# Kernel tuning notes

Measured on AMD Instinct MI355X. Metric: run time of the kernel, lower is better.

The kernel has to match this reference:

```python
import jax, jax.numpy as jnp
import numpy as np

EMB = 256
N = 262144
B = 512
SLOPE = 0.01  # torch LeakyReLU default negative slope


def leaky_relu(x):
    return jnp.where(x >= 0, x, SLOPE * x)


def setup_inputs() -> dict:
    key = jax.random.key(0)
    ks = jax.random.split(key, 10)
    s = 1.0 / np.sqrt(EMB)
    s2 = 1.0 / np.sqrt(2 * EMB)
    return {
        "xg_prev": jax.random.normal(ks[0], (B, EMB), jnp.float32),
        "x": jax.random.normal(ks[1], (N, EMB), jnp.float32),
        "batch_ind": jnp.sort(jax.random.randint(ks[2], (N,), 0, B)),
        "W_mask": jax.random.uniform(ks[3], (EMB, 1), jnp.float32, -s, s),
        "b_mask": jax.random.uniform(ks[4], (1,), jnp.float32, -s, s),
        "W_feat": jax.random.uniform(ks[5], (EMB, EMB), jnp.float32, -s, s),
        "b_feat": jax.random.uniform(ks[6], (EMB,), jnp.float32, -s, s),
        "W_t": jax.random.uniform(ks[7], (2 * EMB, EMB), jnp.float32, -s2, s2),
        "b_t": jax.random.uniform(ks[8], (EMB,), jnp.float32, -s2, s2),
    }


def reference(xg_prev, x, batch_ind, W_mask, b_mask, W_feat, b_feat, W_t, b_t):
    # GlobalAttention pooling (PyG): gate = att_mask(x), feat = att_feat(x)
    gate = (x @ W_mask + b_mask)[:, 0]                      # [N]
    feat = leaky_relu(x @ W_feat + b_feat)                  # [N, EMB]
    # segment-wise stable softmax over gate per graph
    seg_max = jax.ops.segment_max(gate, batch_ind, num_segments=B)  # [B]
    seg_max = jnp.where(jnp.isfinite(seg_max), seg_max, 0.0)
    e = jnp.exp(gate - seg_max[batch_ind])                  # [N]
    denom = jax.ops.segment_sum(e, batch_ind, num_segments=B)      # [B]
    w = e / jnp.maximum(denom[batch_ind], 1e-16)            # [N]
    xg = jax.ops.segment_sum(w[:, None] * feat, batch_ind, num_segments=B)  # [B, EMB]
    # concat -> linear -> leaky_relu -> residual
    h = jnp.concatenate([xg, xg_prev], axis=1)              # [B, 2*EMB]
    out = leaky_relu(h @ W_t + b_t) + xg_prev               # [B, EMB]
    return out
```

## Files before the change

### kernel.cpp

```cpp
#include <hip/hip_runtime.h>
#include <cstdint>
#include <cstddef>

#define NROWS 262144
#define EMB 256
#define NB 512
#define NCOPY 8
#define SLOPE 0.01f

typedef __attribute__((ext_vector_type(8))) short short8;
typedef __attribute__((ext_vector_type(4))) float f32x4;

__device__ __forceinline__ unsigned short f2bf(float f) {
    unsigned u = __float_as_uint(f);
    u += 0x7FFFu + ((u >> 16) & 1u);
    return (unsigned short)(u >> 16);
}

__device__ __forceinline__ short8 pack8(const float4& lo, const float4& hi) {
    short8 s;
    s[0] = (short)f2bf(lo.x); s[1] = (short)f2bf(lo.y);
    s[2] = (short)f2bf(lo.z); s[3] = (short)f2bf(lo.w);
    s[4] = (short)f2bf(hi.x); s[5] = (short)f2bf(hi.y);
    s[6] = (short)f2bf(hi.z); s[7] = (short)f2bf(hi.w);
    return s;
}

__device__ __forceinline__ void gld16f(float* l, const float* g) {
    __builtin_amdgcn_global_load_lds(
        (const __attribute__((address_space(1))) unsigned int*)g,
        (__attribute__((address_space(3))) unsigned int*)l, 16, 0, 0);
}
__device__ __forceinline__ void gld16u(unsigned short* l, const unsigned short* g) {
    __builtin_amdgcn_global_load_lds(
        (const __attribute__((address_space(1))) unsigned int*)g,
        (__attribute__((address_space(3))) unsigned int*)l, 16, 0, 0);
}

__global__ __launch_bounds__(256) void k_init(float4* xgPart4, float4* dPart4) {
    int i = blockIdx.x * 256 + threadIdx.x;
    if (i < NCOPY * NB * EMB / 4) xgPart4[i] = (float4){0.f, 0.f, 0.f, 0.f};
    else dPart4[i - NCOPY * NB * EMB / 4] = (float4){0.f, 0.f, 0.f, 0.f};
}

__global__ __launch_bounds__(256) void k_prep(const float* __restrict__ Wf,
                                              unsigned short* __restrict__ Wt2) {
    int b = blockIdx.x, t = threadIdx.x;
    float v = Wf[(size_t)b * EMB + t];
    Wt2[((size_t)(b >> 3) << 11) + (t << 3) + (b & 7)] = f2bf(v);
}

#define STAGE(B, KT) do {                                                         \
    _Pragma("unroll")                                                             \
    for (int q = 0; q < 2; q++) {                                                 \
        const int i_ = q * 512 + t;                                               \
        const int row_ = i_ >> 3, c_ = i_ & 7;                                    \
        const int cs_ = c_ ^ (row_ & 7);                                          \
        gld16f(&xbuf[B][i_ * 4], x + ((r0 + row_) << 8) + (KT) + (cs_ << 2));     \
    }                                                                             \
    _Pragma("unroll")                                                             \
    for (int q = 0; q < 2; q++) {                                                 \
        const int i_ = q * 512 + t;                                               \
        const int slab_ = i_ >> 8, off_ = i_ & 255;                               \
        gld16u(&bbuf[B][slab_ * 2048 + off_ * 8],                                 \
               Wt2 + (((size_t)((KT) >> 3) + slab_) << 11) + off_ * 8);           \
    }                                                                             \
} while (0)

__global__ __launch_bounds__(512, 4) void k_fused(const float* __restrict__ x,
                                                  const unsigned short* __restrict__ Wt2,
                                                  const float* __restrict__ wm,
                                                  const float* __restrict__ bfeat,
                                                  const int* __restrict__ bind,
                                                  float* __restrict__ dPart,
                                                  float* __restrict__ xgPart) {
    __shared__ float          xbuf[2][128 * 32];
    __shared__ unsigned short bbuf[2][32 * 256];
    __shared__ float wm_s[256];
    __shared__ float w_s[128];
    __shared__ float pxg[2][256];
    __shared__ float pden[2];
    __shared__ int   seg_s[128];
    __shared__ int   segid_s[8];
    __shared__ int   uni_s[8];

    const int t    = threadIdx.x;
    const int lane = t & 63;
    const int w    = t >> 6;
    const int wr   = w >> 1, wc = w & 1;
    const int fr   = lane & 15;
    const int fg   = lane >> 4;
    const size_t r0 = (size_t)blockIdx.x * 128;
    const int cp   = blockIdx.x & (NCOPY - 1);

    if (t < 256) { wm_s[t] = wm[t]; pxg[0][t] = 0.f; pxg[1][t] = 0.f; }
    if (t < 128) seg_s[t] = bind[r0 + t];
    if (t < 2)   pden[t] = 0.f;

    STAGE(0, 0);

    f32x4 acc[2][8];
#pragma unroll
    for (int m = 0; m < 2; m++)
#pragma unroll
        for (int n = 0; n < 8; n++) acc[m][n] = (f32x4){0.f, 0.f, 0.f, 0.f};
    float gp0 = 0.f, gp1 = 0.f;

#pragma unroll
    for (int s = 0; s < 8; s++) {
        const int buf = s & 1;
        if (s < 7) STAGE(buf ^ 1, (s + 1) * 32);
        if (s < 7) asm volatile("s_waitcnt vmcnt(4)" ::: "memory");
        else       asm volatile("s_waitcnt vmcnt(0)" ::: "memory");
        __builtin_amdgcn_sched_barrier(0);
        __builtin_amdgcn_s_barrier();
        __builtin_amdgcn_sched_barrier(0);

        const float* xb = &xbuf[buf][0];
        const unsigned short* bb = &bbuf[buf][0];

        const float4 wa  = *reinterpret_cast<const float4*>(&wm_s[s * 32 + fg * 8]);
        const float4 wbv = *reinterpret_cast<const float4*>(&wm_s[s * 32 + fg * 8 + 4]);
        short8 a0, a1;
        {
            const int r  = wr * 32 + fr;
            const int sl = (fg * 2) ^ (r & 7);
            const float4 lo = *reinterpret_cast<const float4*>(&xb[r * 32 + sl * 4]);
            const float4 hi = *reinterpret_cast<const float4*>(&xb[r * 32 + (sl ^ 1) * 4]);
            gp0 += lo.x * wa.x + lo.y * wa.y + lo.z * wa.z + lo.w * wa.w
                 + hi.x * wbv.x + hi.y * wbv.y + hi.z * wbv.z + hi.w * wbv.w;
            a0 = pack8(lo, hi);
        }
        {
            const int r  = wr * 32 + 16 + fr;
            const int sl = (fg * 2) ^ (r & 7);
            const float4 lo = *reinterpret_cast<const float4*>(&xb[r * 32 + sl * 4]);
            const float4 hi = *reinterpret_cast<const float4*>(&xb[r * 32 + (sl ^ 1) * 4]);
            gp1 += lo.x * wa.x + lo.y * wa.y + lo.z * wa.z + lo.w * wa.w
                 + hi.x * wbv.x + hi.y * wbv.y + hi.z * wbv.z + hi.w * wbv.w;
            a1 = pack8(lo, hi);
        }
#pragma unroll
        for (int n = 0; n < 8; n++) {
            const short8 b = *reinterpret_cast<const short8*>(
                &bb[fg * 2048 + ((wc * 128 + n * 16 + fr) << 3)]);
            acc[0][n] = __builtin_amdgcn_mfma_f32_16x16x32_bf16(a0, b, acc[0][n], 0, 0, 0);
            acc[1][n] = __builtin_amdgcn_mfma_f32_16x16x32_bf16(a1, b, acc[1][n], 0, 0, 0);
        }

        asm volatile("s_waitcnt lgkmcnt(0)" ::: "memory");
        __builtin_amdgcn_sched_barrier(0);
        __builtin_amdgcn_s_barrier();
        __builtin_amdgcn_sched_barrier(0);
    }

    gp0 += __shfl_xor(gp0, 16, 64); gp0 += __shfl_xor(gp0, 32, 64);
    gp1 += __shfl_xor(gp1, 16, 64); gp1 += __shfl_xor(gp1, 32, 64);
    if (wc == 0 && lane < 16) {
        w_s[wr * 32 + lane]      = expf(gp0);
        w_s[wr * 32 + 16 + lane] = expf(gp1);
    }
    if (t < 8) {
        int s0 = seg_s[t * 16], ok = 1;
#pragma unroll
        for (int i = 1; i < 16; i++) ok &= (seg_s[t * 16 + i] == s0);
        segid_s[t] = s0;
        uni_s[t]   = ok;
    }
    __syncthreads();

    const int sid0 = seg_s[0];
    const int sid1 = seg_s[127];

    if (t < 8) {
        if (uni_s[t]) {
            float s = 0.f;
#pragma unroll
            for (int i = 0; i < 16; i++) s += w_s[t * 16 + i];
            const int sid = segid_s[t];
            if (sid == sid0)      atomicAdd(&pden[0], s);
            else if (sid == sid1) atomicAdd(&pden[1], s);
            else atomicAdd(&dPart[cp * NB + sid], s);
        } else {
            for (int i = 0; i < 16; i++) {
                const int sd = seg_s[t * 16 + i];
                const float e = w_s[t * 16 + i];
                if (sd == sid0)      atomicAdd(&pden[0], e);
                else if (sd == sid1) atomicAdd(&pden[1], e);
                else atomicAdd(&dPart[cp * NB + sd], e);
            }
        }
    }

#pragma unroll
    for (int m = 0; m < 2; m++) {
        const int g    = wr * 2 + m;
        const int uni  = uni_s[g];
        const int sid  = segid_s[g];
        const int rowb = wr * 32 + m * 16;
#pragma unroll
        for (int n = 0; n < 8; n++) {
            const int col = wc * 128 + n * 16 + fr;
            const float bia = bfeat[col];
            float vr[4];
#pragma unroll
            for (int r = 0; r < 4; r++) {
                const int row = rowb + fg * 4 + r;
                float v = acc[m][n][r] + bia;
                v = (v >= 0.f) ? v : SLOPE * v;
                vr[r] = v * w_s[row];
            }
            if (uni) {
                float s = vr[0] + vr[1] + vr[2] + vr[3];
                s += __shfl_xor(s, 16, 64);
                s += __shfl_xor(s, 32, 64);
                if (fg == 0) {
                    if (sid == sid0)      atomicAdd(&pxg[0][col], s);
                    else if (sid == sid1) atomicAdd(&pxg[1][col], s);
                    else atomicAdd(&xgPart[((size_t)(cp * NB + sid) << 8) + col], s);
                }
            } else {
#pragma unroll
                for (int r = 0; r < 4; r++) {
                    const int sd = seg_s[rowb + fg * 4 + r];
                    if (sd == sid0)      atomicAdd(&pxg[0][col], vr[r]);
                    else if (sd == sid1) atomicAdd(&pxg[1][col], vr[r]);
                    else atomicAdd(&xgPart[((size_t)(cp * NB + sd) << 8) + col], vr[r]);
                }
            }
        }
    }
    __syncthreads();

    if (t < 256) {
        atomicAdd(&xgPart[((size_t)(cp * NB + sid0) << 8) + t], pxg[0][t]);
    } else if (sid1 != sid0) {
        atomicAdd(&xgPart[((size_t)(cp * NB + sid1) << 8) + (t - 256)], pxg[1][t - 256]);
    }
    if (t == 0) atomicAdd(&dPart[cp * NB + sid0], pden[0]);
    if (t == 1 && sid1 != sid0) atomicAdd(&dPart[cp * NB + sid1], pden[1]);
}

__global__ __launch_bounds__(256) void k_out(const float* __restrict__ xgPart,
                                             const float* __restrict__ dPart,
                                             const float* __restrict__ xgp,
                                             const float* __restrict__ Wtr,
                                             const float* __restrict__ bt,
                                             float* __restrict__ out) {
    __shared__ float h[8][512];
    const int c  = threadIdx.x;
    const int b0 = blockIdx.x * 8;
#pragma unroll
    for (int r = 0; r < 8; r++) {
        const int b = b0 + r;
        float den = 0.f, s = 0.f;
#pragma unroll
        for (int cpy = 0; cpy < NCOPY; cpy++) {
            den += dPart[cpy * NB + b];
            s   += xgPart[((size_t)(cpy * NB + b) << 8) + c];
        }
        h[r][c]       = s / fmaxf(den, 1e-16f);
        h[r][EMB + c] = xgp[(size_t)b * EMB + c];
    }
    __syncthreads();
    float acc[8] = {0.f, 0.f, 0.f, 0.f, 0.f, 0.f, 0.f, 0.f};
    for (int k = 0; k < 2 * EMB; k++) {
        float wv = Wtr[(size_t)k * EMB + c];
#pragma unroll
        for (int r = 0; r < 8; r++) acc[r] += h[r][k] * wv;
    }
#pragma unroll
    for (int r = 0; r < 8; r++) {
        float v = acc[r] + bt[c];
        v = (v >= 0.f) ? v : SLOPE * v;
        out[(size_t)(b0 + r) * EMB + c] = v + xgp[(size_t)(b0 + r) * EMB + c];
    }
}

extern "C" void kernel_launch(void* const* d_in, const int* in_sizes, int n_in,
                              void* d_out, int out_size, void* d_ws, size_t ws_size,
                              hipStream_t stream) {
    const float* xgp  = (const float*)d_in[0];
    const float* x    = (const float*)d_in[1];
    const int*   bind = (const int*)d_in[2];
    const float* Wm   = (const float*)d_in[3];
    const float* Wf   = (const float*)d_in[5];
    const float* bf   = (const float*)d_in[6];
    const float* Wtr  = (const float*)d_in[7];
    const float* bt   = (const float*)d_in[8];
    float* out = (float*)d_out;

    char* ws = (char*)d_ws;
    unsigned short* Wt2    = (unsigned short*)ws;
    float*          dPart  = (float*)(ws + 131072);
    float*          xgPart = (float*)(ws + 131072 + 16384);

    hipLaunchKernelGGL(k_init,  dim3(1028),        dim3(256), 0, stream,
                       (float4*)xgPart, (float4*)dPart);
    hipLaunchKernelGGL(k_prep,  dim3(256),         dim3(256), 0, stream, Wf, Wt2);
    hipLaunchKernelGGL(k_fused, dim3(NROWS / 128), dim3(512), 0, stream,
                       x, Wt2, Wm, bf, bind, dPart, xgPart);
    hipLaunchKernelGGL(k_out,   dim3(NB / 8),      dim3(256), 0, stream,
                       xgPart, dPart, xgp, Wtr, bt, out);
}
```

Before: 142.6 us.

## Load x directly into registers and halve rows per block

The x tile is no longer staged through LDS. Each lane now loads its own A fragment (8 floats per k-step) straight from global memory into registers and prefetches the next step one iteration ahead. The block tile shrinks from 128 to 64 rows, so there are twice as many blocks, and launch bounds rise to 6 blocks per SM to cut LDS and register use and raise occupancy. In exchange, the W tile in LDS is now reused across only 64 rows, so per-row W staging traffic doubles and per-block overhead such as pxg atomics and setup grows.

```diff
diff --git a/kernel.cpp b/kernel.cpp
--- a/kernel.cpp
+++ b/kernel.cpp
@@ -26,11 +26,6 @@
     return s;
 }
 
-__device__ __forceinline__ void gld16f(float* l, const float* g) {
-    __builtin_amdgcn_global_load_lds(
-        (const __attribute__((address_space(1))) unsigned int*)g,
-        (__attribute__((address_space(3))) unsigned int*)l, 16, 0, 0);
-}
 __device__ __forceinline__ void gld16u(unsigned short* l, const unsigned short* g) {
     __builtin_amdgcn_global_load_lds(
         (const __attribute__((address_space(1))) unsigned int*)g,
@@ -50,14 +45,7 @@
     Wt2[((size_t)(b >> 3) << 11) + (t << 3) + (b & 7)] = f2bf(v);
 }
 
-#define STAGE(B, KT) do {                                                         \
-    _Pragma("unroll")                                                             \
-    for (int q = 0; q < 2; q++) {                                                 \
-        const int i_ = q * 512 + t;                                               \
-        const int row_ = i_ >> 3, c_ = i_ & 7;                                    \
-        const int cs_ = c_ ^ (row_ & 7);                                          \
-        gld16f(&xbuf[B][i_ * 4], x + ((r0 + row_) << 8) + (KT) + (cs_ << 2));     \
-    }                                                                             \
+#define STAGE_B(B, KT) do {                                                       \
     _Pragma("unroll")                                                             \
     for (int q = 0; q < 2; q++) {                                                 \
         const int i_ = q * 512 + t;                                               \
@@ -67,22 +55,21 @@
     }                                                                             \
 } while (0)
 
-__global__ __launch_bounds__(512, 4) void k_fused(const float* __restrict__ x,
+__global__ __launch_bounds__(512, 6) void k_fused(const float* __restrict__ x,
                                                   const unsigned short* __restrict__ Wt2,
                                                   const float* __restrict__ wm,
                                                   const float* __restrict__ bfeat,
                                                   const int* __restrict__ bind,
                                                   float* __restrict__ dPart,
                                                   float* __restrict__ xgPart) {
-    __shared__ float          xbuf[2][128 * 32];
     __shared__ unsigned short bbuf[2][32 * 256];
     __shared__ float wm_s[256];
-    __shared__ float w_s[128];
+    __shared__ float w_s[64];
     __shared__ float pxg[2][256];
     __shared__ float pden[2];
-    __shared__ int   seg_s[128];
-    __shared__ int   segid_s[8];
-    __shared__ int   uni_s[8];
+    __shared__ int   seg_s[64];
+    __shared__ int   segid_s[4];
+    __shared__ int   uni_s[4];
 
     const int t    = threadIdx.x;
     const int lane = t & 63;
@@ -90,77 +77,64 @@
     const int wr   = w >> 1, wc = w & 1;
     const int fr   = lane & 15;
     const int fg   = lane >> 4;
-    const size_t r0 = (size_t)blockIdx.x * 128;
+    const size_t r0 = (size_t)blockIdx.x * 64;
     const int cp   = blockIdx.x & (NCOPY - 1);
 
     if (t < 256) { wm_s[t] = wm[t]; pxg[0][t] = 0.f; pxg[1][t] = 0.f; }
-    if (t < 128) seg_s[t] = bind[r0 + t];
-    if (t < 2)   pden[t] = 0.f;
-
-    STAGE(0, 0);
-
-    f32x4 acc[2][8];
-#pragma unroll
-    for (int m = 0; m < 2; m++)
-#pragma unroll
-        for (int n = 0; n < 8; n++) acc[m][n] = (f32x4){0.f, 0.f, 0.f, 0.f};
-    float gp0 = 0.f, gp1 = 0.f;
+    if (t < 64) seg_s[t] = bind[r0 + t];
+    if (t < 2)  pden[t] = 0.f;
+
+    const float* xrow = x + (r0 + wr * 16 + fr) * EMB + fg * 8;
+
+    STAGE_B(0, 0);
+    float4 aLo = *reinterpret_cast<const float4*>(xrow);
+    float4 aHi = *reinterpret_cast<const float4*>(xrow + 4);
+
+    f32x4 acc[8];
+#pragma unroll
+    for (int n = 0; n < 8; n++) acc[n] = (f32x4){0.f, 0.f, 0.f, 0.f};
+    float gp = 0.f;
 
 #pragma unroll
     for (int s = 0; s < 8; s++) {
         const int buf = s & 1;
-        if (s < 7) STAGE(buf ^ 1, (s + 1) * 32);
-        if (s < 7) asm volatile("s_waitcnt vmcnt(4)" ::: "memory");
+        float4 nLo, nHi;
+        if (s < 7) {
+            STAGE_B(buf ^ 1, (s + 1) * 32);
+            nLo = *reinterpret_cast<const float4*>(xrow + (s + 1) * 32);
+            nHi = *reinterpret_cast<const float4*>(xrow + (s + 1) * 32 + 4);
+        }
+        if (s < 7) asm volatile("s_waitcnt vmcnt(6)" ::: "memory");
         else       asm volatile("s_waitcnt vmcnt(0)" ::: "memory");
         __builtin_amdgcn_sched_barrier(0);
         __builtin_amdgcn_s_barrier();
         __builtin_amdgcn_sched_barrier(0);
-
-        const float* xb = &xbuf[buf][0];
-        const unsigned short* bb = &bbuf[buf][0];
 
         const float4 wa  = *reinterpret_cast<const float4*>(&wm_s[s * 32 + fg * 8]);
         const float4 wbv = *reinterpret_cast<const float4*>(&wm_s[s * 32 + fg * 8 + 4]);
-        short8 a0, a1;
-        {
-            const int r  = wr * 32 + fr;
-            const int sl = (fg * 2) ^ (r & 7);
-            const float4 lo = *reinterpret_cast<const float4*>(&xb[r * 32 + sl * 4]);
-            const float4 hi = *reinterpret_cast<const float4*>(&xb[r * 32 + (sl ^ 1) * 4]);
-            gp0 += lo.x * wa.x + lo.y * wa.y + lo.z * wa.z + lo.w * wa.w
-                 + hi.x * wbv.x + hi.y * wbv.y + hi.z * wbv.z + hi.w * wbv.w;
-            a0 = pack8(lo, hi);
-        }
-        {
-            const int r  = wr * 32 + 16 + fr;
-            const int sl = (fg * 2) ^ (r & 7);
-            const float4 lo = *reinterpret_cast<const float4*>(&xb[r * 32 + sl * 4]);
-            const float4 hi = *reinterpret_cast<const float4*>(&xb[r * 32 + (sl ^ 1) * 4]);
-            gp1 += lo.x * wa.x + lo.y * wa.y + lo.z * wa.z + lo.w * wa.w
-                 + hi.x * wbv.x + hi.y * wbv.y + hi.z * wbv.z + hi.w * wbv.w;
-            a1 = pack8(lo, hi);
-        }
+        gp += aLo.x * wa.x + aLo.y * wa.y + aLo.z * wa.z + aLo.w * wa.w
+            + aHi.x * wbv.x + aHi.y * wbv.y + aHi.z * wbv.z + aHi.w * wbv.w;
+        const short8 a = pack8(aLo, aHi);
+        const unsigned short* bb = &bbuf[buf][0];
 #pragma unroll
         for (int n = 0; n < 8; n++) {
             const short8 b = *reinterpret_cast<const short8*>(
                 &bb[fg * 2048 + ((wc * 128 + n * 16 + fr) << 3)]);
-            acc[0][n] = __builtin_amdgcn_mfma_f32_16x16x32_bf16(a0, b, acc[0][n], 0, 0, 0);
-            acc[1][n] = __builtin_amdgcn_mfma_f32_16x16x32_bf16(a1, b, acc[1][n], 0, 0, 0);
+            acc[n] = __builtin_amdgcn_mfma_f32_16x16x32_bf16(a, b, acc[n], 0, 0, 0);
         }
 
         asm volatile("s_waitcnt lgkmcnt(0)" ::: "memory");
         __builtin_amdgcn_sched_barrier(0);
         __builtin_amdgcn_s_barrier();
         __builtin_amdgcn_sched_barrier(0);
-    }
-
-    gp0 += __shfl_xor(gp0, 16, 64); gp0 += __shfl_xor(gp0, 32, 64);
-    gp1 += __shfl_xor(gp1, 16, 64); gp1 += __shfl_xor(gp1, 32, 64);
-    if (wc == 0 && lane < 16) {
-        w_s[wr * 32 + lane]      = expf(gp0);
-        w_s[wr * 32 + 16 + lane] = expf(gp1);
-    }
-    if (t < 8) {
+
+        aLo = nLo; aHi = nHi;
+    }
+
+    gp += __shfl_xor(gp, 16, 64);
+    gp += __shfl_xor(gp, 32, 64);
+    if (wc == 0 && lane < 16) w_s[wr * 16 + lane] = expf(gp);
+    if (t < 4) {
         int s0 = seg_s[t * 16], ok = 1;
 #pragma unroll
         for (int i = 1; i < 16; i++) ok &= (seg_s[t * 16 + i] == s0);
@@ -170,9 +144,9 @@
     __syncthreads();
 
     const int sid0 = seg_s[0];
-    const int sid1 = seg_s[127];
-
-    if (t < 8) {
+    const int sid1 = seg_s[63];
+
+    if (t < 4) {
         if (uni_s[t]) {
             float s = 0.f;
 #pragma unroll
@@ -192,12 +166,11 @@
         }
     }
 
-#pragma unroll
-    for (int m = 0; m < 2; m++) {
-        const int g    = wr * 2 + m;
+    {
+        const int g    = wr;
         const int uni  = uni_s[g];
         const int sid  = segid_s[g];
-        const int rowb = wr * 32 + m * 16;
+        const int rowb = wr * 16;
 #pragma unroll
         for (int n = 0; n < 8; n++) {
             const int col = wc * 128 + n * 16 + fr;
@@ -206,7 +179,7 @@
 #pragma unroll
             for (int r = 0; r < 4; r++) {
                 const int row = rowb + fg * 4 + r;
-                float v = acc[m][n][r] + bia;
+                float v = acc[n][r] + bia;
                 v = (v >= 0.f) ? v : SLOPE * v;
                 vr[r] = v * w_s[row];
             }
@@ -295,11 +268,11 @@
     float*          dPart  = (float*)(ws + 131072);
     float*          xgPart = (float*)(ws + 131072 + 16384);
 
-    hipLaunchKernelGGL(k_init,  dim3(1028),        dim3(256), 0, stream,
+    hipLaunchKernelGGL(k_init,  dim3(1028),       dim3(256), 0, stream,
                        (float4*)xgPart, (float4*)dPart);
-    hipLaunchKernelGGL(k_prep,  dim3(256),         dim3(256), 0, stream, Wf, Wt2);
-    hipLaunchKernelGGL(k_fused, dim3(NROWS / 128), dim3(512), 0, stream,
+    hipLaunchKernelGGL(k_prep,  dim3(256),        dim3(256), 0, stream, Wf, Wt2);
+    hipLaunchKernelGGL(k_fused, dim3(NROWS / 64), dim3(512), 0, stream,
                        x, Wt2, Wm, bf, bind, dPart, xgPart);
-    hipLaunchKernelGGL(k_out,   dim3(NB / 8),      dim3(256), 0, stream,
+    hipLaunchKernelGGL(k_out,   dim3(NB / 8),     dim3(256), 0, stream,
                        xgPart, dPart, xgp, Wtr, bt, out);
 }
```

Result: slower. 161.3 us (+13.1%).

## Stage x through registers with two-ahead prefetch and merge init/prep kernels

Applied to the files above, without the earlier changes.

Replaces the direct global-to-LDS loads of x with register loads that are fetched two k-steps ahead and written into the swizzled LDS buffer one step ahead. The weight tile still uses global_load_lds, and the vmcnt waits are retuned to match. Separately, the zeroing kernel is folded into the weight-prep kernel, which removes one launch. This raises register pressure and adds explicit LDS stores in exchange for a deeper prefetch of the dominant x stream.

```diff
diff --git a/kernel.cpp b/kernel.cpp
--- a/kernel.cpp
+++ b/kernel.cpp
@@ -26,38 +26,28 @@
     return s;
 }
 
-__device__ __forceinline__ void gld16f(float* l, const float* g) {
-    __builtin_amdgcn_global_load_lds(
-        (const __attribute__((address_space(1))) unsigned int*)g,
-        (__attribute__((address_space(3))) unsigned int*)l, 16, 0, 0);
-}
 __device__ __forceinline__ void gld16u(unsigned short* l, const unsigned short* g) {
     __builtin_amdgcn_global_load_lds(
         (const __attribute__((address_space(1))) unsigned int*)g,
         (__attribute__((address_space(3))) unsigned int*)l, 16, 0, 0);
 }
 
-__global__ __launch_bounds__(256) void k_init(float4* xgPart4, float4* dPart4) {
-    int i = blockIdx.x * 256 + threadIdx.x;
-    if (i < NCOPY * NB * EMB / 4) xgPart4[i] = (float4){0.f, 0.f, 0.f, 0.f};
-    else dPart4[i - NCOPY * NB * EMB / 4] = (float4){0.f, 0.f, 0.f, 0.f};
-}
-
 __global__ __launch_bounds__(256) void k_prep(const float* __restrict__ Wf,
-                                              unsigned short* __restrict__ Wt2) {
-    int b = blockIdx.x, t = threadIdx.x;
-    float v = Wf[(size_t)b * EMB + t];
-    Wt2[((size_t)(b >> 3) << 11) + (t << 3) + (b & 7)] = f2bf(v);
-}
-
-#define STAGE(B, KT) do {                                                         \
-    _Pragma("unroll")                                                             \
-    for (int q = 0; q < 2; q++) {                                                 \
-        const int i_ = q * 512 + t;                                               \
-        const int row_ = i_ >> 3, c_ = i_ & 7;                                    \
-        const int cs_ = c_ ^ (row_ & 7);                                          \
-        gld16f(&xbuf[B][i_ * 4], x + ((r0 + row_) << 8) + (KT) + (cs_ << 2));     \
-    }                                                                             \
+                                              unsigned short* __restrict__ Wt2,
+                                              float4* __restrict__ xgPart4,
+                                              float4* __restrict__ dPart4) {
+    const int b = blockIdx.x, t = threadIdx.x;
+    if (b < 256) {
+        float v = Wf[(size_t)b * EMB + t];
+        Wt2[((size_t)(b >> 3) << 11) + (t << 3) + (b & 7)] = f2bf(v);
+    } else {
+        const int i = (b - 256) * 256 + t;
+        if (i < NCOPY * NB * EMB / 4) xgPart4[i] = (float4){0.f, 0.f, 0.f, 0.f};
+        else dPart4[i - NCOPY * NB * EMB / 4] = (float4){0.f, 0.f, 0.f, 0.f};
+    }
+}
+
+#define STAGE_B(B, KT) do {                                                       \
     _Pragma("unroll")                                                             \
     for (int q = 0; q < 2; q++) {                                                 \
         const int i_ = q * 512 + t;                                               \
@@ -97,7 +87,28 @@
     if (t < 128) seg_s[t] = bind[r0 + t];
     if (t < 2)   pden[t] = 0.f;
 
-    STAGE(0, 0);
+    const int row0  = t >> 3, c0 = t & 7;
+    const int wslot = c0 ^ (row0 & 7);
+    const int wb0   = row0 * 32 + wslot * 4;
+    const int wb1   = wb0 + 64 * 32;
+    const float* xsrc0 = x + (r0 + row0) * EMB + c0 * 4;
+    const float* xsrc1 = xsrc0 + (size_t)64 * EMB;
+
+    float4 aLo, aHi, nLo = {}, nHi = {};
+    {
+        float4 z0 = *reinterpret_cast<const float4*>(xsrc0);
+        float4 z1 = *reinterpret_cast<const float4*>(xsrc1);
+        __builtin_amdgcn_sched_barrier(0);
+        STAGE_B(0, 0);
+        __builtin_amdgcn_sched_barrier(0);
+        aLo = *reinterpret_cast<const float4*>(xsrc0 + 32);
+        aHi = *reinterpret_cast<const float4*>(xsrc1 + 32);
+        __builtin_amdgcn_sched_barrier(0);
+        asm volatile("s_waitcnt vmcnt(4)" ::: "memory");
+        __builtin_amdgcn_sched_barrier(0);
+        *reinterpret_cast<float4*>(&xbuf[0][wb0]) = z0;
+        *reinterpret_cast<float4*>(&xbuf[0][wb1]) = z1;
+    }
 
     f32x4 acc[2][8];
 #pragma unroll
@@ -109,9 +120,22 @@
 #pragma unroll
     for (int s = 0; s < 8; s++) {
         const int buf = s & 1;
-        if (s < 7) STAGE(buf ^ 1, (s + 1) * 32);
-        if (s < 7) asm volatile("s_waitcnt vmcnt(4)" ::: "memory");
-        else       asm volatile("s_waitcnt vmcnt(0)" ::: "memory");
+        if (s < 7) STAGE_B(buf ^ 1, (s + 1) * 32);
+        __builtin_amdgcn_sched_barrier(0);
+        if (s < 6) {
+            nLo = *reinterpret_cast<const float4*>(xsrc0 + (s + 2) * 32);
+            nHi = *reinterpret_cast<const float4*>(xsrc1 + (s + 2) * 32);
+        }
+        __builtin_amdgcn_sched_barrier(0);
+        if (s < 6)       asm volatile("s_waitcnt vmcnt(4)" ::: "memory");
+        else if (s == 6) asm volatile("s_waitcnt vmcnt(2)" ::: "memory");
+        else             asm volatile("s_waitcnt vmcnt(0)" ::: "memory");
+        __builtin_amdgcn_sched_barrier(0);
+        if (s < 7) {
+            *reinterpret_cast<float4*>(&xbuf[buf ^ 1][wb0]) = aLo;
+            *reinterpret_cast<float4*>(&xbuf[buf ^ 1][wb1]) = aHi;
+        }
+        asm volatile("s_waitcnt lgkmcnt(0)" ::: "memory");
         __builtin_amdgcn_sched_barrier(0);
         __builtin_amdgcn_s_barrier();
         __builtin_amdgcn_sched_barrier(0);
@@ -152,6 +176,8 @@
         __builtin_amdgcn_sched_barrier(0);
         __builtin_amdgcn_s_barrier();
         __builtin_amdgcn_sched_barrier(0);
+
+        aLo = nLo; aHi = nHi;
     }
 
     gp0 += __shfl_xor(gp0, 16, 64); gp0 += __shfl_xor(gp0, 32, 64);
@@ -204,11 +230,11 @@
             const float bia = bfeat[col];
             float vr[4];
 #pragma unroll
-            for (int r = 0; r < 4; r++) {
-                const int row = rowb + fg * 4 + r;
-                float v = acc[m][n][r] + bia;
+            for (int r2 = 0; r2 < 4; r2++) {
+                const int row = rowb + fg * 4 + r2;
+                float v = acc[m][n][r2] + bia;
                 v = (v >= 0.f) ? v : SLOPE * v;
-                vr[r] = v * w_s[row];
+                vr[r2] = v * w_s[row];
             }
             if (uni) {
                 float s = vr[0] + vr[1] + vr[2] + vr[3];
@@ -221,11 +247,11 @@
                 }
             } else {
 #pragma unroll
-                for (int r = 0; r < 4; r++) {
-                    const int sd = seg_s[rowb + fg * 4 + r];
-                    if (sd == sid0)      atomicAdd(&pxg[0][col], vr[r]);
-                    else if (sd == sid1) atomicAdd(&pxg[1][col], vr[r]);
-                    else atomicAdd(&xgPart[((size_t)(cp * NB + sd) << 8) + col], vr[r]);
+                for (int r2 = 0; r2 < 4; r2++) {
+                    const int sd = seg_s[rowb + fg * 4 + r2];
+                    if (sd == sid0)      atomicAdd(&pxg[0][col], vr[r2]);
+                    else if (sd == sid1) atomicAdd(&pxg[1][col], vr[r2]);
+                    else atomicAdd(&xgPart[((size_t)(cp * NB + sd) << 8) + col], vr[r2]);
                 }
             }
         }
@@ -295,11 +321,10 @@
     float*          dPart  = (float*)(ws + 131072);
     float*          xgPart = (float*)(ws + 131072 + 16384);
 
-    hipLaunchKernelGGL(k_init,  dim3(1028),        dim3(256), 0, stream,
-                       (float4*)xgPart, (float4*)dPart);
-    hipLaunchKernelGGL(k_prep,  dim3(256),         dim3(256), 0, stream, Wf, Wt2);
+    hipLaunchKernelGGL(k_prep,  dim3(256 + 1028), dim3(256), 0, stream,
+                       Wf, Wt2, (float4*)xgPart, (float4*)dPart);
     hipLaunchKernelGGL(k_fused, dim3(NROWS / 128), dim3(512), 0, stream,
                        x, Wt2, Wm, bf, bind, dPart, xgPart);
-    hipLaunchKernelGGL(k_out,   dim3(NB / 8),      dim3(256), 0, stream,
+    hipLaunchKernelGGL(k_out,   dim3(NB / 8),     dim3(256), 0, stream,
                        xgPart, dPart, xgp, Wtr, bt, out);
 }
```

Result: no change. 144.5 us (+1.3%).

## Double row tile to 256 per 1024-thread block and merge init into prep

Applied to the files above, without the earlier changes.

The fused kernel now processes 256 rows per block with 1024 threads (16 waves), so each staged B tile of the bf16 weight matrix is shared by twice as many rows. This halves the weight traffic per row and halves the number of blocks and global atomic flushes. The zero-init kernel is folded into the weight-prep kernel, removing one launch. In exchange, LDS use per block roughly doubles (xbuf grows to 64 KB), which can cut residency and overlap, and launch_bounds(1024,4) may force tight register limits.

```diff
diff --git a/kernel.cpp b/kernel.cpp
--- a/kernel.cpp
+++ b/kernel.cpp
@@ -37,52 +37,52 @@
         (__attribute__((address_space(3))) unsigned int*)l, 16, 0, 0);
 }
 
-__global__ __launch_bounds__(256) void k_init(float4* xgPart4, float4* dPart4) {
-    int i = blockIdx.x * 256 + threadIdx.x;
-    if (i < NCOPY * NB * EMB / 4) xgPart4[i] = (float4){0.f, 0.f, 0.f, 0.f};
-    else dPart4[i - NCOPY * NB * EMB / 4] = (float4){0.f, 0.f, 0.f, 0.f};
-}
-
 __global__ __launch_bounds__(256) void k_prep(const float* __restrict__ Wf,
-                                              unsigned short* __restrict__ Wt2) {
-    int b = blockIdx.x, t = threadIdx.x;
-    float v = Wf[(size_t)b * EMB + t];
-    Wt2[((size_t)(b >> 3) << 11) + (t << 3) + (b & 7)] = f2bf(v);
+                                              unsigned short* __restrict__ Wt2,
+                                              float4* __restrict__ xgPart4,
+                                              float4* __restrict__ dPart4) {
+    const int b = blockIdx.x, t = threadIdx.x;
+    if (b < 256) {
+        float v = Wf[(size_t)b * EMB + t];
+        Wt2[((size_t)(b >> 3) << 11) + (t << 3) + (b & 7)] = f2bf(v);
+    } else {
+        const int i = (b - 256) * 256 + t;
+        if (i < NCOPY * NB * EMB / 4) xgPart4[i] = (float4){0.f, 0.f, 0.f, 0.f};
+        else dPart4[i - NCOPY * NB * EMB / 4] = (float4){0.f, 0.f, 0.f, 0.f};
+    }
 }
 
 #define STAGE(B, KT) do {                                                         \
     _Pragma("unroll")                                                             \
     for (int q = 0; q < 2; q++) {                                                 \
-        const int i_ = q * 512 + t;                                               \
+        const int i_ = q * 1024 + t;                                              \
         const int row_ = i_ >> 3, c_ = i_ & 7;                                    \
         const int cs_ = c_ ^ (row_ & 7);                                          \
         gld16f(&xbuf[B][i_ * 4], x + ((r0 + row_) << 8) + (KT) + (cs_ << 2));     \
     }                                                                             \
-    _Pragma("unroll")                                                             \
-    for (int q = 0; q < 2; q++) {                                                 \
-        const int i_ = q * 512 + t;                                               \
-        const int slab_ = i_ >> 8, off_ = i_ & 255;                               \
+    {                                                                             \
+        const int slab_ = t >> 8, off_ = t & 255;                                 \
         gld16u(&bbuf[B][slab_ * 2048 + off_ * 8],                                 \
                Wt2 + (((size_t)((KT) >> 3) + slab_) << 11) + off_ * 8);           \
     }                                                                             \
 } while (0)
 
-__global__ __launch_bounds__(512, 4) void k_fused(const float* __restrict__ x,
-                                                  const unsigned short* __restrict__ Wt2,
-                                                  const float* __restrict__ wm,
-                                                  const float* __restrict__ bfeat,
-                                                  const int* __restrict__ bind,
-                                                  float* __restrict__ dPart,
-                                                  float* __restrict__ xgPart) {
-    __shared__ float          xbuf[2][128 * 32];
+__global__ __launch_bounds__(1024, 4) void k_fused(const float* __restrict__ x,
+                                                   const unsigned short* __restrict__ Wt2,
+                                                   const float* __restrict__ wm,
+                                                   const float* __restrict__ bfeat,
+                                                   const int* __restrict__ bind,
+                                                   float* __restrict__ dPart,
+                                                   float* __restrict__ xgPart) {
+    __shared__ float          xbuf[2][256 * 32];
     __shared__ unsigned short bbuf[2][32 * 256];
     __shared__ float wm_s[256];
-    __shared__ float w_s[128];
+    __shared__ float w_s[256];
     __shared__ float pxg[2][256];
     __shared__ float pden[2];
-    __shared__ int   seg_s[128];
-    __shared__ int   segid_s[8];
-    __shared__ int   uni_s[8];
+    __shared__ int   seg_s[256];
+    __shared__ int   segid_s[16];
+    __shared__ int   uni_s[16];
 
     const int t    = threadIdx.x;
     const int lane = t & 63;
@@ -90,12 +90,16 @@
     const int wr   = w >> 1, wc = w & 1;
     const int fr   = lane & 15;
     const int fg   = lane >> 4;
-    const size_t r0 = (size_t)blockIdx.x * 128;
+    const size_t r0 = (size_t)blockIdx.x * 256;
     const int cp   = blockIdx.x & (NCOPY - 1);
 
-    if (t < 256) { wm_s[t] = wm[t]; pxg[0][t] = 0.f; pxg[1][t] = 0.f; }
-    if (t < 128) seg_s[t] = bind[r0 + t];
-    if (t < 2)   pden[t] = 0.f;
+    if (t < 256) {
+        wm_s[t] = wm[t];
+        pxg[0][t] = 0.f;
+        pxg[1][t] = 0.f;
+        seg_s[t] = bind[r0 + t];
+    }
+    if (t < 2) pden[t] = 0.f;
 
     STAGE(0, 0);
 
@@ -110,8 +114,9 @@
     for (int s = 0; s < 8; s++) {
         const int buf = s & 1;
         if (s < 7) STAGE(buf ^ 1, (s + 1) * 32);
-        if (s < 7) asm volatile("s_waitcnt vmcnt(4)" ::: "memory");
-        else       asm volatile("s_waitcnt vmcnt(0)" ::: "memory");
+        if (s == 0)     asm volatile("s_waitcnt vmcnt(3) lgkmcnt(0)" ::: "memory");
+        else if (s < 7) asm volatile("s_waitcnt vmcnt(3)" ::: "memory");
+        else            asm volatile("s_waitcnt vmcnt(0)" ::: "memory");
         __builtin_amdgcn_sched_barrier(0);
         __builtin_amdgcn_s_barrier();
         __builtin_amdgcn_sched_barrier(0);
@@ -160,7 +165,7 @@
         w_s[wr * 32 + lane]      = expf(gp0);
         w_s[wr * 32 + 16 + lane] = expf(gp1);
     }
-    if (t < 8) {
+    if (t < 16) {
         int s0 = seg_s[t * 16], ok = 1;
 #pragma unroll
         for (int i = 1; i < 16; i++) ok &= (seg_s[t * 16 + i] == s0);
@@ -170,9 +175,9 @@
     __syncthreads();
 
     const int sid0 = seg_s[0];
-    const int sid1 = seg_s[127];
-
-    if (t < 8) {
+    const int sid1 = seg_s[255];
+
+    if (t < 16) {
         if (uni_s[t]) {
             float s = 0.f;
 #pragma unroll
@@ -204,11 +209,11 @@
             const float bia = bfeat[col];
             float vr[4];
 #pragma unroll
-            for (int r = 0; r < 4; r++) {
-                const int row = rowb + fg * 4 + r;
-                float v = acc[m][n][r] + bia;
+            for (int r2 = 0; r2 < 4; r2++) {
+                const int row = rowb + fg * 4 + r2;
+                float v = acc[m][n][r2] + bia;
                 v = (v >= 0.f) ? v : SLOPE * v;
-                vr[r] = v * w_s[row];
+                vr[r2] = v * w_s[row];
             }
             if (uni) {
                 float s = vr[0] + vr[1] + vr[2] + vr[3];
@@ -221,11 +226,11 @@
                 }
             } else {
 #pragma unroll
-                for (int r = 0; r < 4; r++) {
-                    const int sd = seg_s[rowb + fg * 4 + r];
-                    if (sd == sid0)      atomicAdd(&pxg[0][col], vr[r]);
-                    else if (sd == sid1) atomicAdd(&pxg[1][col], vr[r]);
-                    else atomicAdd(&xgPart[((size_t)(cp * NB + sd) << 8) + col], vr[r]);
+                for (int r2 = 0; r2 < 4; r2++) {
+                    const int sd = seg_s[rowb + fg * 4 + r2];
+                    if (sd == sid0)      atomicAdd(&pxg[0][col], vr[r2]);
+                    else if (sd == sid1) atomicAdd(&pxg[1][col], vr[r2]);
+                    else atomicAdd(&xgPart[((size_t)(cp * NB + sd) << 8) + col], vr[r2]);
                 }
             }
         }
@@ -234,11 +239,14 @@
 
     if (t < 256) {
         atomicAdd(&xgPart[((size_t)(cp * NB + sid0) << 8) + t], pxg[0][t]);
-    } else if (sid1 != sid0) {
-        atomicAdd(&xgPart[((size_t)(cp * NB + sid1) << 8) + (t - 256)], pxg[1][t - 256]);
-    }
-    if (t == 0) atomicAdd(&dPart[cp * NB + sid0], pden[0]);
-    if (t == 1 && sid1 != sid0) atomicAdd(&dPart[cp * NB + sid1], pden[1]);
+    } else if (t < 512) {
+        if (sid1 != sid0)
+            atomicAdd(&xgPart[((size_t)(cp * NB + sid1) << 8) + (t - 256)], pxg[1][t - 256]);
+    } else if (t == 512) {
+        atomicAdd(&dPart[cp * NB + sid0], pden[0]);
+    } else if (t == 513) {
+        if (sid1 != sid0) atomicAdd(&dPart[cp * NB + sid1], pden[1]);
+    }
 }
 
 __global__ __launch_bounds__(256) void k_out(const float* __restrict__ xgPart,
@@ -295,11 +303,10 @@
     float*          dPart  = (float*)(ws + 131072);
     float*          xgPart = (float*)(ws + 131072 + 16384);
 
-    hipLaunchKernelGGL(k_init,  dim3(1028),        dim3(256), 0, stream,
-                       (float4*)xgPart, (float4*)dPart);
-    hipLaunchKernelGGL(k_prep,  dim3(256),         dim3(256), 0, stream, Wf, Wt2);
-    hipLaunchKernelGGL(k_fused, dim3(NROWS / 128), dim3(512), 0, stream,
+    hipLaunchKernelGGL(k_prep,  dim3(256 + 1028), dim3(256),  0, stream,
+                       Wf, Wt2, (float4*)xgPart, (float4*)dPart);
+    hipLaunchKernelGGL(k_fused, dim3(NROWS / 256), dim3(1024), 0, stream,
                        x, Wt2, Wm, bf, bind, dPart, xgPart);
-    hipLaunchKernelGGL(k_out,   dim3(NB / 8),      dim3(256), 0, stream,
+    hipLaunchKernelGGL(k_out,   dim3(NB / 8),     dim3(256),  0, stream,
                        xgPart, dPart, xgp, Wtr, bt, out);
 }
```

Measured after the change: 143.5 us. About the same (+0.6%).
